# Kernel tuning notes

Measured on AMD Instinct MI355X. Metric: run time of the kernel, lower is better.

## Reference

```python
import jax, jax.numpy as jnp
import numpy as np

GRID_SIZE = 0.04   # matches init_kwargs grid_size
AXIS_CAP = 32      # max voxel bins per axis (1/0.04 = 25 < 32); keeps keys in int32 range


def setup_inputs() -> dict:
    key = jax.random.key(0)
    k1, k2 = jax.random.split(key)
    N, C = 1_000_000, 64
    coord = jax.random.uniform(k1, (N, 3), dtype=jnp.float32)   # points in unit cube
    feat = jax.random.normal(k2, (N, C), dtype=jnp.float32)
    # cumulative per-batch point counts (pointops offset convention), 4 equal batches
    offset = jnp.array([N // 4, N // 2, 3 * N // 4, N], dtype=jnp.int32)
    return {"coord": coord, "feat": feat, "offset": offset}


def reference(coord, feat, offset):
    N = coord.shape[0]
    B = offset.shape[0]
    # batch id per point from cumulative offsets
    batch = jnp.searchsorted(offset, jnp.arange(N, dtype=offset.dtype), side='right')  # [N]
    batch = batch.astype(jnp.int32)
    # voxelize_helper: start = per-batch min coord (start=None path)
    start = jax.ops.segment_min(coord, batch, num_segments=B)            # [B,3]
    vox = jnp.floor((coord - start[batch]) / GRID_SIZE).astype(jnp.int32)  # [N,3]
    # fused (batch, voxel) key; batches never share keys
    vkey = ((batch * AXIS_CAP + vox[:, 0]) * AXIS_CAP + vox[:, 1]) * AXIS_CAP + vox[:, 2]
    # sorted cluster indices + CSR-style segment ids
    order = jnp.argsort(vkey)                                            # sorted_cluster_indices
    skey = vkey[order]
    new_seg = jnp.concatenate([jnp.zeros((1,), jnp.int32),
                               (skey[1:] != skey[:-1]).astype(jnp.int32)])
    seg = jnp.cumsum(new_seg)                                            # [N] segment id per sorted point
    n_vox = seg[-1] + 1                                                  # actual number of voxels (traced)
    # segment_csr(coord[order], reduce='mean')
    counts = jax.ops.segment_sum(jnp.ones((N,), coord.dtype), seg, num_segments=N)  # [N] padded
    coord_out = jax.ops.segment_sum(coord[order], seg, num_segments=N) / jnp.maximum(counts, 1.0)[:, None]
    # segment_csr(feat[order], reduce='max')
    feat_out = jax.ops.segment_max(feat[order], seg, num_segments=N)
    valid = jnp.arange(N) < n_vox                                        # [N] pad mask
    coord_out = jnp.where(valid[:, None], coord_out, 0.0)
    feat_out = jnp.where(valid[:, None], feat_out, 0.0)
    # batch[idx_ptr[:-1]] -> batch of first point in each segment, then batch2offset
    batch_out = jax.ops.segment_min(batch[order], seg, num_segments=N)
    batch_out = jnp.where(valid, batch_out, B)                           # padded rows -> bucket B
    per_batch = jax.ops.segment_sum(jnp.ones((N,), jnp.int32), batch_out, num_segments=B + 1)[:B]
    offset_out = jnp.cumsum(per_batch)                                   # [B]
    # outputs padded to N rows; first n_vox rows are the real voxels
    return coord_out, feat_out, offset_out, n_vox
```

## Files before the change

kernel.cpp:

```cpp
#include <hip/hip_runtime.h>
#include <hip/hip_bf16.h>
#include <cstdint>

#define AXIS_CAP 32
#define GRID_SIZE_F 0.04f
#define BINS_PER_BATCH (AXIS_CAP * AXIS_CAP * AXIS_CAP)
#define SCAN_TPB 256
#define BINS_PER_THREAD 4
#define BINS_PER_BLOCK (SCAN_TPB * BINS_PER_THREAD)

typedef float f32x4 __attribute__((ext_vector_type(4)));

__device__ __forceinline__ int point_batch(int i, const int* offs, int B) {
    int b = 0;
    for (int k = 0; k < B; ++k) b += (offs[k] <= i);
    return b;
}

__global__ void init_kernel(uint32_t* binCount, int nbins, int* startBits, int B) {
    int i = blockIdx.x * blockDim.x + threadIdx.x;
    int stride = gridDim.x * blockDim.x;
    for (int v = i; v < nbins; v += stride) binCount[v] = 0;
    if (i < 3 * B) startBits[i] = 0x7F800000;
}

__global__ __launch_bounds__(256) void batch_min4_kernel(
        const float* __restrict__ coord, const int* __restrict__ offs,
        int B, int N, int* __restrict__ startBits) {
    __shared__ int smin[12];
    if (threadIdx.x < 12) smin[threadIdx.x] = 0x7F800000;
    __syncthreads();

    int o0 = offs[0];
    int o1 = (B > 1) ? offs[1] : o0;
    int o2 = (B > 2) ? offs[2] : o1;

    float m[4][3];
#pragma unroll
    for (int bb = 0; bb < 4; ++bb)
#pragma unroll
        for (int d = 0; d < 3; ++d) m[bb][d] = INFINITY;

    int gid = blockIdx.x * blockDim.x + threadIdx.x;
    int stride = gridDim.x * blockDim.x;
    for (int i = gid; i < N; i += stride) {
        float x = coord[(size_t)i * 3 + 0];
        float y = coord[(size_t)i * 3 + 1];
        float z = coord[(size_t)i * 3 + 2];
        int b = (i >= o0) + (i >= o1) + (i >= o2);
#pragma unroll
        for (int bb = 0; bb < 4; ++bb) {
            bool sel = (bb == b);
            m[bb][0] = fminf(m[bb][0], sel ? x : INFINITY);
            m[bb][1] = fminf(m[bb][1], sel ? y : INFINITY);
            m[bb][2] = fminf(m[bb][2], sel ? z : INFINITY);
        }
    }

#pragma unroll
    for (int bb = 0; bb < 4; ++bb)
#pragma unroll
        for (int d = 0; d < 3; ++d) {
            float v = m[bb][d];
            for (int off = 32; off > 0; off >>= 1)
                v = fminf(v, __shfl_xor(v, off));
            m[bb][d] = v;
        }

    if ((threadIdx.x & 63) == 0) {
#pragma unroll
        for (int bb = 0; bb < 4; ++bb)
#pragma unroll
            for (int d = 0; d < 3; ++d)
                atomicMin(&smin[bb * 3 + d], __float_as_int(m[bb][d]));
    }
    __syncthreads();
    if (threadIdx.x < 12 && (threadIdx.x / 3) < B)
        atomicMin(&startBits[threadIdx.x], smin[threadIdx.x]);
}

__global__ void batch_min_generic_kernel(const float* __restrict__ coord,
                                         const int* __restrict__ offs,
                                         int B, int N, int* startBits) {
    int i = blockIdx.x * blockDim.x + threadIdx.x;
    if (i >= N) return;
    int b = point_batch(i, offs, B);
    for (int d = 0; d < 3; ++d) {
        float c = coord[(size_t)i * 3 + d];
        atomicMin(&startBits[b * 3 + d], __float_as_int(c));
    }
}

__global__ void keys_count_kernel(const float* __restrict__ coord,
                                  const int* __restrict__ offs,
                                  const int* __restrict__ startBits,
                                  int B, int N,
                                  uint32_t* __restrict__ keys,
                                  uint32_t* __restrict__ rank,
                                  uint32_t* __restrict__ binCount) {
    int i = blockIdx.x * blockDim.x + threadIdx.x;
    if (i >= N) return;
    int b = point_batch(i, offs, B);
    int v[3];
    for (int d = 0; d < 3; ++d) {
        float s = __int_as_float(startBits[b * 3 + d]);
        float q = (coord[(size_t)i * 3 + d] - s) / GRID_SIZE_F;
        int vi = (int)floorf(q);
        vi = vi < 0 ? 0 : (vi > AXIS_CAP - 1 ? AXIS_CAP - 1 : vi);
        v[d] = vi;
    }
    uint32_t key = ((uint32_t)b * AXIS_CAP + v[0]) * AXIS_CAP * AXIS_CAP
                 + (uint32_t)v[1] * AXIS_CAP + v[2];
    keys[i] = key;
    rank[i] = atomicAdd(&binCount[key], 1u);
}

__global__ void scan1_kernel(const uint32_t* __restrict__ binCount,
                             uint32_t* __restrict__ binStart,
                             uint32_t* __restrict__ binSeg,
                             uint32_t* __restrict__ blockCnt,
                             uint32_t* __restrict__ blockOcc) {
    __shared__ uint32_t sC[SCAN_TPB], sO[SCAN_TPB];
    int t = threadIdx.x;
    int base = blockIdx.x * BINS_PER_BLOCK + t * BINS_PER_THREAD;
    uint32_t c[BINS_PER_THREAD];
    uint32_t tc = 0, to = 0;
#pragma unroll
    for (int j = 0; j < BINS_PER_THREAD; ++j) {
        c[j] = binCount[base + j];
        tc += c[j];
        to += (c[j] > 0u);
    }
    sC[t] = tc; sO[t] = to;
    __syncthreads();
    for (int off = 1; off < SCAN_TPB; off <<= 1) {
        uint32_t a = 0, b2 = 0;
        if (t >= off) { a = sC[t - off]; b2 = sO[t - off]; }
        __syncthreads();
        sC[t] += a; sO[t] += b2;
        __syncthreads();
    }
    uint32_t exC = sC[t] - tc;
    uint32_t exO = sO[t] - to;
#pragma unroll
    for (int j = 0; j < BINS_PER_THREAD; ++j) {
        binStart[base + j] = exC;
        binSeg[base + j] = exO;
        exC += c[j];
        exO += (c[j] > 0u);
    }
    if (t == SCAN_TPB - 1) {
        blockCnt[blockIdx.x] = sC[t];
        blockOcc[blockIdx.x] = sO[t];
    }
}

__global__ void scan2_kernel(uint32_t* blockCnt, uint32_t* blockOcc,
                             uint32_t* totals, int nb) {
    __shared__ uint32_t sC[SCAN_TPB], sO[SCAN_TPB];
    int t = threadIdx.x;
    uint32_t c = (t < nb) ? blockCnt[t] : 0u;
    uint32_t o = (t < nb) ? blockOcc[t] : 0u;
    sC[t] = c; sO[t] = o;
    __syncthreads();
    for (int off = 1; off < SCAN_TPB; off <<= 1) {
        uint32_t a = 0, b2 = 0;
        if (t >= off) { a = sC[t - off]; b2 = sO[t - off]; }
        __syncthreads();
        sC[t] += a; sO[t] += b2;
        __syncthreads();
    }
    if (t < nb) { blockCnt[t] = sC[t] - c; blockOcc[t] = sO[t] - o; }
    if (t == SCAN_TPB - 1) { totals[0] = sO[t]; totals[1] = sC[t]; }
}

__global__ void scan3_kernel(uint32_t* __restrict__ binStart,
                             uint32_t* __restrict__ binSeg,
                             const uint32_t* __restrict__ blockCnt,
                             const uint32_t* __restrict__ blockOcc) {
    int t = threadIdx.x;
    int base = blockIdx.x * BINS_PER_BLOCK + t * BINS_PER_THREAD;
    uint32_t oc = blockCnt[blockIdx.x];
    uint32_t oo = blockOcc[blockIdx.x];
#pragma unroll
    for (int j = 0; j < BINS_PER_THREAD; ++j) {
        binStart[base + j] += oc;
        binSeg[base + j] += oo;
    }
}

__global__ void scatter_kernel(const uint32_t* __restrict__ keys,
                               const uint32_t* __restrict__ rank,
                               const uint32_t* __restrict__ binStart,
                               uint32_t* __restrict__ pointIdx, int N) {
    int i = blockIdx.x * blockDim.x + threadIdx.x;
    if (i >= N) return;
    uint32_t pos = binStart[keys[i]] + rank[i];
    pointIdx[pos] = (uint32_t)i;
}

__global__ __launch_bounds__(64) void reduce_kernel(
        const float* __restrict__ coord, const float* __restrict__ feat,
        const uint32_t* __restrict__ binCount,
        const uint32_t* __restrict__ binStart,
        const uint32_t* __restrict__ binSeg,
        const uint32_t* __restrict__ pointIdx,
        float* __restrict__ out, int N, int C) {
    int bin = blockIdx.x;
    uint32_t cnt = binCount[bin];
    if (cnt == 0u) return;
    uint32_t st = binStart[bin];
    uint32_t seg = binSeg[bin];
    int lane = threadIdx.x;
    float* feat_out = out + (size_t)N * 3;

    float sx = 0.f, sy = 0.f, sz = 0.f;

    if ((C & 3) == 0 && C <= 64) {
        int g = lane >> 4;
        int l4 = lane & 15;
        int q4 = C >> 2;
        f32x4 mx = {-INFINITY, -INFINITY, -INFINITY, -INFINITY};
        for (uint32_t base = 0; base < cnt; base += 64) {
            uint32_t nchunk = min(64u, cnt - base);
            bool valid = lane < (int)nchunk;
            uint32_t myIdx = valid ? pointIdx[st + base + lane] : 0u;
            if (valid) {
                sx += coord[(size_t)myIdx * 3 + 0];
                sy += coord[(size_t)myIdx * 3 + 1];
                sz += coord[(size_t)myIdx * 3 + 2];
            }
            for (uint32_t p = (uint32_t)g; p < nchunk; p += 4) {
                uint32_t idx = __shfl(myIdx, (int)p);
                if (l4 < q4) {
                    const f32x4* row = (const f32x4*)(feat + (size_t)idx * C);
                    f32x4 v = row[l4];
                    mx.x = fmaxf(mx.x, v.x);
                    mx.y = fmaxf(mx.y, v.y);
                    mx.z = fmaxf(mx.z, v.z);
                    mx.w = fmaxf(mx.w, v.w);
                }
            }
        }
        mx.x = fmaxf(mx.x, __shfl_xor(mx.x, 16));
        mx.y = fmaxf(mx.y, __shfl_xor(mx.y, 16));
        mx.z = fmaxf(mx.z, __shfl_xor(mx.z, 16));
        mx.w = fmaxf(mx.w, __shfl_xor(mx.w, 16));
        mx.x = fmaxf(mx.x, __shfl_xor(mx.x, 32));
        mx.y = fmaxf(mx.y, __shfl_xor(mx.y, 32));
        mx.z = fmaxf(mx.z, __shfl_xor(mx.z, 32));
        mx.w = fmaxf(mx.w, __shfl_xor(mx.w, 32));
        if (g == 0 && l4 < q4)
            ((f32x4*)(feat_out + (size_t)seg * C))[l4] = mx;
    } else {
        for (uint32_t p = lane; p < cnt; p += 64) {
            uint32_t idx = pointIdx[st + p];
            sx += coord[(size_t)idx * 3 + 0];
            sy += coord[(size_t)idx * 3 + 1];
            sz += coord[(size_t)idx * 3 + 2];
        }
        for (int c = lane; c < C; c += 64) {
            float m = -INFINITY;
            for (uint32_t p = 0; p < cnt; ++p) {
                uint32_t idx = pointIdx[st + p];
                m = fmaxf(m, feat[(size_t)idx * C + c]);
            }
            feat_out[(size_t)seg * C + c] = m;
        }
    }

    for (int off = 32; off > 0; off >>= 1) {
        sx += __shfl_xor(sx, off);
        sy += __shfl_xor(sy, off);
        sz += __shfl_xor(sz, off);
    }
    if (lane == 0) {
        float inv = 1.0f / (float)cnt;
        out[(size_t)seg * 3 + 0] = sx * inv;
        out[(size_t)seg * 3 + 1] = sy * inv;
        out[(size_t)seg * 3 + 2] = sz * inv;
    }
}

__global__ void pad_kernel(float* __restrict__ out,
                           const uint32_t* __restrict__ totals, int N, int C) {
    uint32_t nvox = totals[0];
    size_t gid = (size_t)blockIdx.x * blockDim.x + threadIdx.x;
    size_t stride = (size_t)gridDim.x * blockDim.x;
    float* featBase = out + (size_t)N * 3;
    f32x4 z4 = {0.f, 0.f, 0.f, 0.f};
    if ((C & 3) == 0) {
        f32x4* f4 = (f32x4*)featBase;
        size_t r4 = (size_t)C / 4;
        size_t v0 = (size_t)nvox * r4, v1 = (size_t)N * r4;
        for (size_t v = v0 + gid; v < v1; v += stride)
            __builtin_nontemporal_store(z4, &f4[v]);
    } else {
        size_t e0 = (size_t)nvox * C, e1 = (size_t)N * C;
        for (size_t e = e0 + gid; e < e1; e += stride)
            __builtin_nontemporal_store(0.f, &featBase[e]);
    }
    size_t c0 = (size_t)nvox * 3, c1 = (size_t)N * 3;
    for (size_t e = c0 + gid; e < c1; e += stride)
        __builtin_nontemporal_store(0.f, &out[e]);
}

__global__ void finalize_kernel(const uint32_t* __restrict__ binSeg,
                                const uint32_t* __restrict__ totals,
                                float* __restrict__ out, int B, int N, int C) {
    int t = threadIdx.x;
    uint32_t nvox = totals[0];
    float* tail = out + (size_t)N * 3 + (size_t)N * C;
    if (t < B) {
        uint32_t v = (t == B - 1) ? nvox
                                  : binSeg[(size_t)(t + 1) * BINS_PER_BATCH];
        tail[t] = (float)v;
    }
    if (t == 0) tail[B] = (float)nvox;
}

extern "C" void kernel_launch(void* const* d_in, const int* in_sizes, int n_in,
                              void* d_out, int out_size, void* d_ws, size_t ws_size,
                              hipStream_t stream) {
    const float* coord = (const float*)d_in[0];
    const float* feat  = (const float*)d_in[1];
    const int*   offs  = (const int*)d_in[2];
    float* out = (float*)d_out;

    int N = in_sizes[0] / 3;
    int C = in_sizes[1] / N;
    int B = in_sizes[2];
    int NBINS = B * BINS_PER_BATCH;
    int NB1 = NBINS / BINS_PER_BLOCK;

    uint8_t* w = (uint8_t*)d_ws;
    uint32_t* binCount = (uint32_t*)w;              w += (size_t)NBINS * 4;
    uint32_t* binStart = (uint32_t*)w;              w += (size_t)NBINS * 4;
    uint32_t* binSeg   = (uint32_t*)w;              w += (size_t)NBINS * 4;
    uint32_t* blockCnt = (uint32_t*)w;              w += (size_t)NB1 * 4;
    uint32_t* blockOcc = (uint32_t*)w;              w += (size_t)NB1 * 4;
    uint32_t* totals   = (uint32_t*)w;              w += 2 * 4;
    int*      startBits= (int*)w;                   w += (size_t)3 * B * 4 + 8;
    uint32_t* keys     = (uint32_t*)w;              w += (size_t)N * 4;
    uint32_t* rank     = (uint32_t*)w;              w += (size_t)N * 4;
    uint32_t* pointIdx = (uint32_t*)w;

    int ptBlocks = (N + 255) / 256;

    init_kernel<<<512, 256, 0, stream>>>(binCount, NBINS, startBits, B);
    if (B <= 4) {
        batch_min4_kernel<<<1024, 256, 0, stream>>>(coord, offs, B, N, startBits);
    } else {
        batch_min_generic_kernel<<<ptBlocks, 256, 0, stream>>>(coord, offs, B, N,
                                                               startBits);
    }
    keys_count_kernel<<<ptBlocks, 256, 0, stream>>>(coord, offs, startBits, B, N,
                                                    keys, rank, binCount);
    scan1_kernel<<<NB1, SCAN_TPB, 0, stream>>>(binCount, binStart, binSeg,
                                               blockCnt, blockOcc);
    scan2_kernel<<<1, SCAN_TPB, 0, stream>>>(blockCnt, blockOcc, totals, NB1);
    scan3_kernel<<<NB1, SCAN_TPB, 0, stream>>>(binStart, binSeg, blockCnt, blockOcc);
    scatter_kernel<<<ptBlocks, 256, 0, stream>>>(keys, rank, binStart, pointIdx, N);
    reduce_kernel<<<NBINS, 64, 0, stream>>>(coord, feat, binCount, binStart,
                                            binSeg, pointIdx, out, N, C);
    pad_kernel<<<2048, 256, 0, stream>>>(out, totals, N, C);
    finalize_kernel<<<1, 64, 0, stream>>>(binSeg, totals, out, B, N, C);
}
```

Baseline: 230.6 us.

## Fuse padding and finalize into reduce/scatter, pack key+rank, specialize key kernel

Removes the separate pad and finalize kernels: zero-padding is distributed across the reduce kernel's blocks and offset/nvox tail writes move into the scatter kernel. Keys and ranks are packed into one uint2 array so scatter does a single 8-byte load. A specialized keys/count kernel for B<=4 keeps per-batch starts in registers and processes four points per thread. This saves launches and memory passes, at the cost of every reduce block (including empty bins) now doing padding work.

```diff
diff --git a/kernel.cpp b/kernel.cpp
--- a/kernel.cpp
+++ b/kernel.cpp
@@ -8,6 +8,7 @@
 #define SCAN_TPB 256
 #define BINS_PER_THREAD 4
 #define BINS_PER_BLOCK (SCAN_TPB * BINS_PER_THREAD)
+#define KC_PPT 4
 
 typedef float f32x4 __attribute__((ext_vector_type(4)));
 
@@ -91,13 +92,55 @@
     }
 }
 
-__global__ void keys_count_kernel(const float* __restrict__ coord,
-                                  const int* __restrict__ offs,
-                                  const int* __restrict__ startBits,
-                                  int B, int N,
-                                  uint32_t* __restrict__ keys,
-                                  uint32_t* __restrict__ rank,
-                                  uint32_t* __restrict__ binCount) {
+__global__ __launch_bounds__(256) void keys_count4_kernel(
+        const float* __restrict__ coord, const int* __restrict__ offs,
+        const int* __restrict__ startBits, int B, int N,
+        uint2* __restrict__ kr, uint32_t* __restrict__ binCount) {
+    int o0 = offs[0];
+    int o1 = (B > 1) ? offs[1] : o0;
+    int o2 = (B > 2) ? offs[2] : o1;
+    float s00 = __int_as_float(startBits[0]);
+    float s01 = __int_as_float(startBits[1]);
+    float s02 = __int_as_float(startBits[2]);
+    float s10 = (B > 1) ? __int_as_float(startBits[3]) : 0.f;
+    float s11 = (B > 1) ? __int_as_float(startBits[4]) : 0.f;
+    float s12 = (B > 1) ? __int_as_float(startBits[5]) : 0.f;
+    float s20 = (B > 2) ? __int_as_float(startBits[6]) : 0.f;
+    float s21 = (B > 2) ? __int_as_float(startBits[7]) : 0.f;
+    float s22 = (B > 2) ? __int_as_float(startBits[8]) : 0.f;
+    float s30 = (B > 3) ? __int_as_float(startBits[9]) : 0.f;
+    float s31 = (B > 3) ? __int_as_float(startBits[10]) : 0.f;
+    float s32 = (B > 3) ? __int_as_float(startBits[11]) : 0.f;
+
+    int i0 = blockIdx.x * (256 * KC_PPT) + threadIdx.x;
+#pragma unroll
+    for (int j = 0; j < KC_PPT; ++j) {
+        int i = i0 + j * 256;
+        if (i >= N) continue;
+        float x = coord[(size_t)i * 3 + 0];
+        float y = coord[(size_t)i * 3 + 1];
+        float z = coord[(size_t)i * 3 + 2];
+        int b = (i >= o0) + (i >= o1) + (i >= o2);
+        float sx = (b == 0) ? s00 : (b == 1) ? s10 : (b == 2) ? s20 : s30;
+        float sy = (b == 0) ? s01 : (b == 1) ? s11 : (b == 2) ? s21 : s31;
+        float sz = (b == 0) ? s02 : (b == 1) ? s12 : (b == 2) ? s22 : s32;
+        int vx = (int)floorf((x - sx) / GRID_SIZE_F);
+        int vy = (int)floorf((y - sy) / GRID_SIZE_F);
+        int vz = (int)floorf((z - sz) / GRID_SIZE_F);
+        vx = vx < 0 ? 0 : (vx > AXIS_CAP - 1 ? AXIS_CAP - 1 : vx);
+        vy = vy < 0 ? 0 : (vy > AXIS_CAP - 1 ? AXIS_CAP - 1 : vy);
+        vz = vz < 0 ? 0 : (vz > AXIS_CAP - 1 ? AXIS_CAP - 1 : vz);
+        uint32_t key = ((uint32_t)b * AXIS_CAP + vx) * AXIS_CAP * AXIS_CAP
+                     + (uint32_t)vy * AXIS_CAP + vz;
+        uint32_t r = atomicAdd(&binCount[key], 1u);
+        kr[i] = make_uint2(key, r);
+    }
+}
+
+__global__ void keys_count_generic_kernel(
+        const float* __restrict__ coord, const int* __restrict__ offs,
+        const int* __restrict__ startBits, int B, int N,
+        uint2* __restrict__ kr, uint32_t* __restrict__ binCount) {
     int i = blockIdx.x * blockDim.x + threadIdx.x;
     if (i >= N) return;
     int b = point_batch(i, offs, B);
@@ -111,8 +154,8 @@
     }
     uint32_t key = ((uint32_t)b * AXIS_CAP + v[0]) * AXIS_CAP * AXIS_CAP
                  + (uint32_t)v[1] * AXIS_CAP + v[2];
-    keys[i] = key;
-    rank[i] = atomicAdd(&binCount[key], 1u);
+    uint32_t r = atomicAdd(&binCount[key], 1u);
+    kr[i] = make_uint2(key, r);
 }
 
 __global__ void scan1_kernel(const uint32_t* __restrict__ binCount,
@@ -189,14 +232,27 @@
     }
 }
 
-__global__ void scatter_kernel(const uint32_t* __restrict__ keys,
-                               const uint32_t* __restrict__ rank,
+__global__ void scatter_kernel(const uint2* __restrict__ kr,
                                const uint32_t* __restrict__ binStart,
-                               uint32_t* __restrict__ pointIdx, int N) {
+                               uint32_t* __restrict__ pointIdx, int N,
+                               const uint32_t* __restrict__ binSeg,
+                               const uint32_t* __restrict__ totals,
+                               float* __restrict__ out, int B, int C) {
     int i = blockIdx.x * blockDim.x + threadIdx.x;
+    if (blockIdx.x == 0 && threadIdx.x <= (unsigned)B) {
+        uint32_t nvox = totals[0];
+        float* tail = out + (size_t)N * 3 + (size_t)N * C;
+        if (threadIdx.x < (unsigned)B) {
+            uint32_t v = (threadIdx.x == (unsigned)(B - 1))
+                             ? nvox
+                             : binSeg[(size_t)(threadIdx.x + 1) * BINS_PER_BATCH];
+            tail[threadIdx.x] = (float)v;
+        }
+        if (threadIdx.x == 0) tail[B] = (float)nvox;
+    }
     if (i >= N) return;
-    uint32_t pos = binStart[keys[i]] + rank[i];
-    pointIdx[pos] = (uint32_t)i;
+    uint2 k = kr[i];
+    pointIdx[binStart[k.x] + k.y] = (uint32_t)i;
 }
 
 __global__ __launch_bounds__(64) void reduce_kernel(
@@ -205,118 +261,114 @@
         const uint32_t* __restrict__ binStart,
         const uint32_t* __restrict__ binSeg,
         const uint32_t* __restrict__ pointIdx,
+        const uint32_t* __restrict__ totals,
         float* __restrict__ out, int N, int C) {
     int bin = blockIdx.x;
     uint32_t cnt = binCount[bin];
-    if (cnt == 0u) return;
-    uint32_t st = binStart[bin];
-    uint32_t seg = binSeg[bin];
     int lane = threadIdx.x;
     float* feat_out = out + (size_t)N * 3;
 
-    float sx = 0.f, sy = 0.f, sz = 0.f;
-
-    if ((C & 3) == 0 && C <= 64) {
-        int g = lane >> 4;
-        int l4 = lane & 15;
-        int q4 = C >> 2;
-        f32x4 mx = {-INFINITY, -INFINITY, -INFINITY, -INFINITY};
-        for (uint32_t base = 0; base < cnt; base += 64) {
-            uint32_t nchunk = min(64u, cnt - base);
-            bool valid = lane < (int)nchunk;
-            uint32_t myIdx = valid ? pointIdx[st + base + lane] : 0u;
-            if (valid) {
-                sx += coord[(size_t)myIdx * 3 + 0];
-                sy += coord[(size_t)myIdx * 3 + 1];
-                sz += coord[(size_t)myIdx * 3 + 2];
-            }
-            for (uint32_t p = (uint32_t)g; p < nchunk; p += 4) {
-                uint32_t idx = __shfl(myIdx, (int)p);
-                if (l4 < q4) {
-                    const f32x4* row = (const f32x4*)(feat + (size_t)idx * C);
-                    f32x4 v = row[l4];
-                    mx.x = fmaxf(mx.x, v.x);
-                    mx.y = fmaxf(mx.y, v.y);
-                    mx.z = fmaxf(mx.z, v.z);
-                    mx.w = fmaxf(mx.w, v.w);
+    if (cnt != 0u) {
+        uint32_t st = binStart[bin];
+        uint32_t seg = binSeg[bin];
+        float sx = 0.f, sy = 0.f, sz = 0.f;
+
+        if ((C & 3) == 0 && C <= 64) {
+            int g = lane >> 4;
+            int l4 = lane & 15;
+            int q4 = C >> 2;
+            f32x4 mx = {-INFINITY, -INFINITY, -INFINITY, -INFINITY};
+            for (uint32_t base = 0; base < cnt; base += 64) {
+                uint32_t nchunk = min(64u, cnt - base);
+                bool valid = lane < (int)nchunk;
+                uint32_t myIdx = valid ? pointIdx[st + base + lane] : 0u;
+                if (valid) {
+                    sx += coord[(size_t)myIdx * 3 + 0];
+                    sy += coord[(size_t)myIdx * 3 + 1];
+                    sz += coord[(size_t)myIdx * 3 + 2];
+                }
+                for (uint32_t p = (uint32_t)g; p < nchunk; p += 4) {
+                    uint32_t idx = __shfl(myIdx, (int)p);
+                    if (l4 < q4) {
+                        const f32x4* row = (const f32x4*)(feat + (size_t)idx * C);
+                        f32x4 v = row[l4];
+                        mx.x = fmaxf(mx.x, v.x);
+                        mx.y = fmaxf(mx.y, v.y);
+                        mx.z = fmaxf(mx.z, v.z);
+                        mx.w = fmaxf(mx.w, v.w);
+                    }
                 }
             }
-        }
-        mx.x = fmaxf(mx.x, __shfl_xor(mx.x, 16));
-        mx.y = fmaxf(mx.y, __shfl_xor(mx.y, 16));
-        mx.z = fmaxf(mx.z, __shfl_xor(mx.z, 16));
-        mx.w = fmaxf(mx.w, __shfl_xor(mx.w, 16));
-        mx.x = fmaxf(mx.x, __shfl_xor(mx.x, 32));
-        mx.y = fmaxf(mx.y, __shfl_xor(mx.y, 32));
-        mx.z = fmaxf(mx.z, __shfl_xor(mx.z, 32));
-        mx.w = fmaxf(mx.w, __shfl_xor(mx.w, 32));
-        if (g == 0 && l4 < q4)
-            ((f32x4*)(feat_out + (size_t)seg * C))[l4] = mx;
+            mx.x = fmaxf(mx.x, __shfl_xor(mx.x, 16));
+            mx.y = fmaxf(mx.y, __shfl_xor(mx.y, 16));
+            mx.z = fmaxf(mx.z, __shfl_xor(mx.z, 16));
+            mx.w = fmaxf(mx.w, __shfl_xor(mx.w, 16));
+            mx.x = fmaxf(mx.x, __shfl_xor(mx.x, 32));
+            mx.y = fmaxf(mx.y, __shfl_xor(mx.y, 32));
+            mx.z = fmaxf(mx.z, __shfl_xor(mx.z, 32));
+            mx.w = fmaxf(mx.w, __shfl_xor(mx.w, 32));
+            if (g == 0 && l4 < q4)
+                ((f32x4*)(feat_out + (size_t)seg * C))[l4] = mx;
+        } else {
+            for (uint32_t p = lane; p < cnt; p += 64) {
+                uint32_t idx = pointIdx[st + p];
+                sx += coord[(size_t)idx * 3 + 0];
+                sy += coord[(size_t)idx * 3 + 1];
+                sz += coord[(size_t)idx * 3 + 2];
+            }
+            for (int c = lane; c < C; c += 64) {
+                float m = -INFINITY;
+                for (uint32_t p = 0; p < cnt; ++p) {
+                    uint32_t idx = pointIdx[st + p];
+                    m = fmaxf(m, feat[(size_t)idx * C + c]);
+                }
+                feat_out[(size_t)seg * C + c] = m;
+            }
+        }
+
+        for (int off = 32; off > 0; off >>= 1) {
+            sx += __shfl_xor(sx, off);
+            sy += __shfl_xor(sy, off);
+            sz += __shfl_xor(sz, off);
+        }
+        if (lane == 0) {
+            float inv = 1.0f / (float)cnt;
+            out[(size_t)seg * 3 + 0] = sx * inv;
+            out[(size_t)seg * 3 + 1] = sy * inv;
+            out[(size_t)seg * 3 + 2] = sz * inv;
+        }
+    }
+
+    uint32_t nvox = totals[0];
+    uint32_t nb = gridDim.x;
+    if ((C & 3) == 0) {
+        f32x4 z4 = {0.f, 0.f, 0.f, 0.f};
+        size_t q4r = (size_t)(C >> 2);
+        size_t quadsTotal = (size_t)(N - (int)nvox) * q4r;
+        size_t chunk = (quadsTotal + nb - 1) / nb;
+        size_t q0 = (size_t)bin * chunk;
+        size_t q1 = min(q0 + chunk, quadsTotal);
+        f32x4* padBase = (f32x4*)(feat_out + (size_t)nvox * C);
+        for (size_t q = q0 + lane; q < q1; q += 64)
+            __builtin_nontemporal_store(z4, &padBase[q]);
     } else {
-        for (uint32_t p = lane; p < cnt; p += 64) {
-            uint32_t idx = pointIdx[st + p];
-            sx += coord[(size_t)idx * 3 + 0];
-            sy += coord[(size_t)idx * 3 + 1];
-            sz += coord[(size_t)idx * 3 + 2];
-        }
-        for (int c = lane; c < C; c += 64) {
-            float m = -INFINITY;
-            for (uint32_t p = 0; p < cnt; ++p) {
-                uint32_t idx = pointIdx[st + p];
-                m = fmaxf(m, feat[(size_t)idx * C + c]);
-            }
-            feat_out[(size_t)seg * C + c] = m;
-        }
-    }
-
-    for (int off = 32; off > 0; off >>= 1) {
-        sx += __shfl_xor(sx, off);
-        sy += __shfl_xor(sy, off);
-        sz += __shfl_xor(sz, off);
-    }
-    if (lane == 0) {
-        float inv = 1.0f / (float)cnt;
-        out[(size_t)seg * 3 + 0] = sx * inv;
-        out[(size_t)seg * 3 + 1] = sy * inv;
-        out[(size_t)seg * 3 + 2] = sz * inv;
-    }
-}
-
-__global__ void pad_kernel(float* __restrict__ out,
-                           const uint32_t* __restrict__ totals, int N, int C) {
-    uint32_t nvox = totals[0];
-    size_t gid = (size_t)blockIdx.x * blockDim.x + threadIdx.x;
-    size_t stride = (size_t)gridDim.x * blockDim.x;
-    float* featBase = out + (size_t)N * 3;
-    f32x4 z4 = {0.f, 0.f, 0.f, 0.f};
-    if ((C & 3) == 0) {
-        f32x4* f4 = (f32x4*)featBase;
-        size_t r4 = (size_t)C / 4;
-        size_t v0 = (size_t)nvox * r4, v1 = (size_t)N * r4;
-        for (size_t v = v0 + gid; v < v1; v += stride)
-            __builtin_nontemporal_store(z4, &f4[v]);
-    } else {
-        size_t e0 = (size_t)nvox * C, e1 = (size_t)N * C;
-        for (size_t e = e0 + gid; e < e1; e += stride)
-            __builtin_nontemporal_store(0.f, &featBase[e]);
-    }
-    size_t c0 = (size_t)nvox * 3, c1 = (size_t)N * 3;
-    for (size_t e = c0 + gid; e < c1; e += stride)
-        __builtin_nontemporal_store(0.f, &out[e]);
-}
-
-__global__ void finalize_kernel(const uint32_t* __restrict__ binSeg,
-                                const uint32_t* __restrict__ totals,
-                                float* __restrict__ out, int B, int N, int C) {
-    int t = threadIdx.x;
-    uint32_t nvox = totals[0];
-    float* tail = out + (size_t)N * 3 + (size_t)N * C;
-    if (t < B) {
-        uint32_t v = (t == B - 1) ? nvox
-                                  : binSeg[(size_t)(t + 1) * BINS_PER_BATCH];
-        tail[t] = (float)v;
-    }
-    if (t == 0) tail[B] = (float)nvox;
+        size_t eTotal = (size_t)(N - (int)nvox) * C;
+        size_t chunk = (eTotal + nb - 1) / nb;
+        size_t e0 = (size_t)bin * chunk;
+        size_t e1 = min(e0 + chunk, eTotal);
+        float* padBase = feat_out + (size_t)nvox * C;
+        for (size_t e = e0 + lane; e < e1; e += 64)
+            __builtin_nontemporal_store(0.f, &padBase[e]);
+    }
+    {
+        size_t cTotal = (size_t)(N - (int)nvox) * 3;
+        size_t chunk = (cTotal + nb - 1) / nb;
+        size_t e0 = (size_t)bin * chunk;
+        size_t e1 = min(e0 + chunk, cTotal);
+        float* cBase = out + (size_t)nvox * 3;
+        for (size_t e = e0 + lane; e < e1; e += 64)
+            __builtin_nontemporal_store(0.f, &cBase[e]);
+    }
 }
 
 extern "C" void kernel_launch(void* const* d_in, const int* in_sizes, int n_in,
@@ -341,28 +393,30 @@
     uint32_t* blockOcc = (uint32_t*)w;              w += (size_t)NB1 * 4;
     uint32_t* totals   = (uint32_t*)w;              w += 2 * 4;
     int*      startBits= (int*)w;                   w += (size_t)3 * B * 4 + 8;
-    uint32_t* keys     = (uint32_t*)w;              w += (size_t)N * 4;
-    uint32_t* rank     = (uint32_t*)w;              w += (size_t)N * 4;
+    uint2*    kr       = (uint2*)w;                 w += (size_t)N * 8;
     uint32_t* pointIdx = (uint32_t*)w;
 
     int ptBlocks = (N + 255) / 256;
+    int kcBlocks = (N + 256 * KC_PPT - 1) / (256 * KC_PPT);
 
     init_kernel<<<512, 256, 0, stream>>>(binCount, NBINS, startBits, B);
     if (B <= 4) {
         batch_min4_kernel<<<1024, 256, 0, stream>>>(coord, offs, B, N, startBits);
+        keys_count4_kernel<<<kcBlocks, 256, 0, stream>>>(coord, offs, startBits,
+                                                         B, N, kr, binCount);
     } else {
         batch_min_generic_kernel<<<ptBlocks, 256, 0, stream>>>(coord, offs, B, N,
                                                                startBits);
-    }
-    keys_count_kernel<<<ptBlocks, 256, 0, stream>>>(coord, offs, startBits, B, N,
-                                                    keys, rank, binCount);
+        keys_count_generic_kernel<<<ptBlocks, 256, 0, stream>>>(coord, offs,
+                                                                startBits, B, N,
+                                                                kr, binCount);
+    }
     scan1_kernel<<<NB1, SCAN_TPB, 0, stream>>>(binCount, binStart, binSeg,
                                                blockCnt, blockOcc);
     scan2_kernel<<<1, SCAN_TPB, 0, stream>>>(blockCnt, blockOcc, totals, NB1);
     scan3_kernel<<<NB1, SCAN_TPB, 0, stream>>>(binStart, binSeg, blockCnt, blockOcc);
-    scatter_kernel<<<ptBlocks, 256, 0, stream>>>(keys, rank, binStart, pointIdx, N);
+    scatter_kernel<<<ptBlocks, 256, 0, stream>>>(kr, binStart, pointIdx, N,
+                                                 binSeg, totals, out, B, C);
     reduce_kernel<<<NBINS, 64, 0, stream>>>(coord, feat, binCount, binStart,
-                                            binSeg, pointIdx, out, N, C);
-    pad_kernel<<<2048, 256, 0, stream>>>(out, totals, N, C);
-    finalize_kernel<<<1, 64, 0, stream>>>(binSeg, totals, out, B, N, C);
-}
+                                            binSeg, pointIdx, totals, out, N, C);
+}
```

After: 207.1 us. 1.11x faster.
